# Optimization experiments

Hardware: AMD Instinct MI355X
Metric: run time of the kernel (lower is better)

## Reference

```python
import jax, jax.numpy as jnp
import numpy as np

R_CUTOFF = 5.0
BASIS = 8
NMAX = 8
NSPECIES = 3
EMBED = 16


def _chebyshev_basis(r, r_cutoff, basis_size):
    fc = jnp.where(r < r_cutoff, 0.5 * jnp.cos(jnp.pi * r / r_cutoff) + 0.5, 0.0)
    x = 2.0 * (r / r_cutoff) ** 2 - 1.0
    polys = [jnp.ones_like(x), x]
    for n in range(2, basis_size):
        polys.append(2.0 * x * polys[-1] - polys[-2])
    basis = jnp.stack(polys[:basis_size], axis=-1)  # [E, basis]
    return 0.5 * (basis + 1.0) * fc[:, None]


def setup_inputs() -> dict:
    key = jax.random.key(0)
    ks = jax.random.split(key, 12)
    N, K = 20000, 32
    E = N * K
    positions = jax.random.normal(ks[0], (N, 3), dtype=jnp.float32)
    species = jax.random.randint(ks[1], (N,), 0, NSPECIES, dtype=jnp.int32)
    magmoms = jax.random.normal(ks[2], (N, 3), dtype=jnp.float32)
    # i-major edge list: exactly K edges per atom, grouped by center atom.
    i_idx = jnp.repeat(jnp.arange(N, dtype=jnp.int32), K)
    j_idx = jax.random.randint(ks[3], (E,), 0, N, dtype=jnp.int32)
    edge_index = jnp.stack([i_idx, j_idx], axis=0)
    shifts = jnp.zeros((E, 3), dtype=jnp.float32)
    rb_coefficients = 0.1 * jax.random.normal(ks[4], (NSPECIES * NSPECIES, NMAX, BASIS), dtype=jnp.float32)
    species_embedding = 0.1 * jax.random.normal(ks[5], (NSPECIES, EMBED), dtype=jnp.float32)
    struct_dim = NMAX + NMAX * (NMAX + 1)  # 80
    mag_dim = 3 + 7 * NMAX + 3 * NMAX * NMAX  # 251
    return {
        'positions': positions, 'species': species, 'magmoms': magmoms,
        'edge_index': edge_index, 'shifts': shifts,
        'rb_coefficients': rb_coefficients, 'species_embedding': species_embedding,
        'struct_shift': jnp.zeros(struct_dim, jnp.float32),
        'struct_scale': jnp.ones(struct_dim, jnp.float32),
        'mag_shift': jnp.zeros(mag_dim, jnp.float32),
        'mag_scale': jnp.ones(mag_dim, jnp.float32),
        'atomic_energy_shift': 0.1 * jax.random.normal(ks[6], (NSPECIES,), dtype=jnp.float32),
        'w_struct': 0.05 * jax.random.normal(ks[7], (EMBED + struct_dim,), dtype=jnp.float32),
        'b_struct': 0.05 * jax.random.normal(ks[8], (1,), dtype=jnp.float32),
        'w_mag': 0.05 * jax.random.normal(ks[9], (EMBED + mag_dim,), dtype=jnp.float32),
        'b_mag': 0.05 * jax.random.normal(ks[10], (1,), dtype=jnp.float32),
    }


def _forward(positions, magmoms, shifts, rb_coefficients, species_embedding,
             struct_shift, struct_scale, mag_shift, mag_scale, atomic_energy_shift,
             w_struct, b_struct, w_mag, b_mag, species, edge_index):
    N = positions.shape[0]
    E = edge_index.shape[1]
    K = E // N  # regular neighbor count (edge list is i-major)
    i_idx, j_idx = edge_index[0], edge_index[1]
    r_ij = positions[j_idx] - positions[i_idx] + shifts          # [E,3]
    dist = jnp.linalg.norm(r_ij, axis=-1)                        # [E]
    f_k = _chebyshev_basis(dist, R_CUTOFF, BASIS)                # [E,basis]
    pair_idx = species[i_idx] * NSPECIES + species[j_idx]
    phi = jnp.einsum('enk,ek->en', rb_coefficients[pair_idx], f_k)  # [E,n]
    seg = lambda x: jax.ops.segment_sum(x, i_idx, num_segments=N)
    d = jnp.maximum(dist, 1e-8)[:, None]
    r_hat = r_ij / d
    # --- structural descriptors ---
    d_radial = seg(phi)                                          # [N,n]
    P = seg(phi[:, :, None] * r_hat[:, None, :])                 # [N,n,3]
    PP = jnp.einsum('ina,ima->inm', P, P)
    tu = np.triu_indices(NMAX)
    d_ang_l1 = PP[:, tu[0], tu[1]]
    eye3 = jnp.eye(3, dtype=r_ij.dtype)
    traceless = r_hat[:, :, None] * r_hat[:, None, :] - eye3 / 3.0  # [E,3,3]
    Q = seg(phi[:, :, None, None] * traceless[:, None, :, :])       # [N,n,3,3]
    Qf = Q.reshape(N, NMAX, 9)
    QQ = jnp.einsum('ina,ima->inm', Qf, Qf)
    d_ang_l2 = QQ[:, tu[0], tu[1]]
    desc_struct = jnp.concatenate([d_radial, d_ang_l1, d_ang_l2], axis=-1)
    # --- magnetic descriptors ---
    u = jnp.sum(magmoms * magmoms, axis=-1)                      # [N]
    m_norm = jnp.linalg.norm(magmoms, axis=-1, keepdims=True)
    m_dir = jnp.where(m_norm > 1e-8, magmoms / jnp.maximum(m_norm, 1e-8), 0.0)
    M = seg(phi[:, :, None] * m_dir[j_idx][:, None, :])          # [N,n,3]
    # A_{nm}(i) = sum_{a<b within atom i's edge block} phi_n(a) phi_m(b) (r_a x r_b)
    phi_g = phi.reshape(N, K, NMAX)
    r_g = r_ij.reshape(N, K, 3)
    cross = jnp.cross(r_g[:, :, None, :], r_g[:, None, :, :])    # [N,K,K,3]
    mask = jnp.triu(jnp.ones((K, K), dtype=phi.dtype), k=1)
    tmp = jnp.einsum('iabd,ab,ibm->iamd', cross, mask, phi_g)    # [N,K,3,n]
    A = jnp.einsum('ian,iamd->inmd', phi_g, tmp)                 # [N,n,n,3]
    d_amp = jnp.stack([u, u ** 2, u ** 3], axis=-1)
    d_iso = jnp.sum(m_dir[:, None, :] * M, axis=-1)              # [N,n]
    Qm = jnp.einsum('anij,aj->ani', Q, m_dir)
    d_sia = jnp.sum(m_dir[:, None, :] * Qm, axis=-1)
    mQ = jnp.einsum('ai,amij->amj', m_dir, Q)
    d_sae = jnp.einsum('amj,anj->amn', mQ, M).reshape(N, -1)
    m_cross_M = jnp.cross(jnp.broadcast_to(m_dir[:, None, :], M.shape), M)
    d_dmi = jnp.einsum('inmd,imd->inm', A, m_cross_M).reshape(N, -1)
    u_col = u[:, None]
    d_amp_mix = jnp.concatenate([u_col * d_iso, u_col * d_sia, u_col * d_dmi], axis=-1)
    u_j = u[j_idx]
    d_nbr_amp = seg(phi * u_j[:, None])
    W = seg(phi[:, :, None] * (u_j[:, None] * m_dir[j_idx])[:, None, :])
    d_nbr_amp_ex = jnp.sum(m_dir[:, None, :] * W, axis=-1)
    d_nbr_amp_ex_mix = u_col * d_nbr_amp_ex
    desc_mag = jnp.concatenate([d_amp, d_iso, d_sia, d_sae, d_dmi, d_amp_mix,
                                d_nbr_amp, d_nbr_amp_ex, d_nbr_amp_ex_mix], axis=-1)
    # --- scaling + linear readout heads + per-species shift ---
    ds = (desc_struct - struct_shift) / struct_scale
    dm = (desc_mag - mag_shift) / mag_scale
    emb = species_embedding[species]
    e_struct = jnp.concatenate([emb, ds], axis=-1) @ w_struct + b_struct[0]
    e_mag = jnp.concatenate([emb, dm], axis=-1) @ w_mag + b_mag[0]
    return e_struct + e_mag + atomic_energy_shift[species]        # [N]


def reference(positions, species, magmoms, edge_index, shifts, rb_coefficients,
              species_embedding, struct_shift, struct_scale, mag_shift, mag_scale,
              atomic_energy_shift, w_struct, b_struct, w_mag, b_mag):
    return _forward(positions, magmoms, shifts, rb_coefficients, species_embedding,
                    struct_shift, struct_scale, mag_shift, mag_scale, atomic_energy_shift,
                    w_struct, b_struct, w_mag, b_mag, species, edge_index)
```

## Files before the change

kernel.cpp:

```cpp
#include <hip/hip_runtime.h>

#define NSPEC  3
#define EMBEDD 16
#define KMAX   32
#define RCUT   5.0f
#define PADR   36

__constant__ int TUN[36] = {0,0,0,0,0,0,0,0, 1,1,1,1,1,1,1, 2,2,2,2,2,2, 3,3,3,3,3, 4,4,4,4, 5,5,5, 6,6, 7};
__constant__ int TUM[36] = {0,1,2,3,4,5,6,7, 1,2,3,4,5,6,7, 2,3,4,5,6,7, 3,4,5,6,7, 4,5,6,7, 5,6,7, 6,7, 7};


template<int CTRL, int RMASK, bool BC>
__device__ __forceinline__ float dpp_mov0(float x) {
    return __int_as_float(__builtin_amdgcn_update_dpp(
        0, __float_as_int(x), CTRL, RMASK, 0xF, BC));
}
__device__ __forceinline__ float prefix32(float x) {
    x += dpp_mov0<0x111, 0xF, true >(x);
    x += dpp_mov0<0x112, 0xF, true >(x);
    x += dpp_mov0<0x114, 0xF, true >(x);
    x += dpp_mov0<0x118, 0xF, true >(x);
    x += dpp_mov0<0x142, 0xA, false>(x);
    return x;
}
__device__ __forceinline__ float swz_xor16(float x) {
    return __int_as_float(__builtin_amdgcn_ds_swizzle(__float_as_int(x), 0x401F));
}
__device__ __forceinline__ float red_k4(float x) {
    x += dpp_mov0<0x128, 0xF, true>(x);
    x += swz_xor16(x);
    return x;
}
__device__ __forceinline__ float red32(float x) {
    x += dpp_mov0<0x121, 0xF, true>(x);
    x += dpp_mov0<0x122, 0xF, true>(x);
    x += dpp_mov0<0x124, 0xF, true>(x);
    x += dpp_mov0<0x128, 0xF, true>(x);
    x += swz_xor16(x);
    return x;
}

struct __align__(16) AtomLds {
    float phiT[8 * PADR];
    float tT[8 * PADR];
    float rhx[KMAX], rhy[KMAX], rhz[KMAX];
    float mdx[KMAX], mdy[KMAX], mdz[KMAX];
    float uj[KMAX];
    float P[24], Q[48], M[24], W[24], mQ[24];
};

__global__ __launch_bounds__(256)
void magpot_setup(const float* __restrict__ sshift, const float* __restrict__ sscale,
                  const float* __restrict__ mshift, const float* __restrict__ mscale,
                  const float* __restrict__ wstruct, const float* __restrict__ bstruct,
                  const float* __restrict__ wmag, const float* __restrict__ bmag,
                  float* __restrict__ ws)
{
    __shared__ float red[4];
    const int t = threadIdx.x;
    float c = 0.0f;
    for (int idx = t; idx < 80; idx += 256) {
        const float w = wstruct[16 + idx] / sscale[idx];
        ws[idx] = w;
        c += w * sshift[idx];
    }
    for (int idx = t; idx < 251; idx += 256) {
        const float w = wmag[16 + idx] / mscale[idx];
        ws[80 + idx] = w;
        c += w * mshift[idx];
    }
    if (t < EMBEDD) ws[332 + t] = wstruct[t] + wmag[t];
    #pragma unroll
    for (int d = 1; d <= 32; d <<= 1) c += __shfl_xor(c, d, 64);
    if ((t & 63) == 0) red[t >> 6] = c;
    __syncthreads();
    if (t == 0) ws[331] = bstruct[0] + bmag[0] - (red[0] + red[1] + red[2] + red[3]);
}

__global__ __launch_bounds__(256)
void magpot_main(const float* __restrict__ pos,
                 const int*   __restrict__ species,
                 const float* __restrict__ mag,
                 const int*   __restrict__ eidx,
                 const float* __restrict__ shifts,
                 const float* __restrict__ rb,
                 const float* __restrict__ semb,
                 const float* __restrict__ aes,
                 const float* __restrict__ ws,
                 float* __restrict__ out,
                 int N, int E, int K)
{
    __shared__ AtomLds lds[8];

    const int lane64 = threadIdx.x & 63;
    const int wv     = threadIdx.x >> 6;
    const int h      = lane64 >> 5;
    const int s      = lane64 & 31;
    const int ea     = 31 - s;
    const int i      = blockIdx.x * 8 + wv * 2 + h;
    const bool valid = (i < N);
    const int isafe  = valid ? i : 0;
    AtomLds& L = lds[wv * 2 + h];

    const float* wm = ws + 80;

    const float pix = pos[3*isafe+0], piy = pos[3*isafe+1], piz = pos[3*isafe+2];
    const int   spi = species[isafe];
    const float mgx = mag[3*isafe+0], mgy = mag[3*isafe+1], mgz = mag[3*isafe+2];
    const float u_i = mgx*mgx + mgy*mgy + mgz*mgz;
    const float mn_i = sqrtf(u_i);
    const float mi_inv = (mn_i > 1e-8f) ? (1.0f / mn_i) : 0.0f;
    const float mix = mgx*mi_inv, miy = mgy*mi_inv, miz = mgz*mi_inv;

    float phi[8];
    float rx = 0.0f, ry = 0.0f, rz = 0.0f;
    #pragma unroll
    for (int n = 0; n < 8; ++n) phi[n] = 0.0f;

    if (ea < K) {
        const int e = isafe * K + ea;
        const int j = eidx[E + e];
        rx = pos[3*j+0] - pix + shifts[3*e+0];
        ry = pos[3*j+1] - piy + shifts[3*e+1];
        rz = pos[3*j+2] - piz + shifts[3*e+2];
        const float dist = sqrtf(rx*rx + ry*ry + rz*rz);
        const float fc = (dist < RCUT)
            ? (0.5f * __builtin_amdgcn_cosf(dist * 0.1f) + 0.5f)
            : 0.0f;
        const float xr = dist * (1.0f/RCUT);
        const float x  = 2.0f * xr * xr - 1.0f;
        float f[8];
        {
            float Tm2 = 1.0f, Tm1 = x;
            f[0] = 0.5f * (Tm2 + 1.0f) * fc;
            f[1] = 0.5f * (Tm1 + 1.0f) * fc;
            #pragma unroll
            for (int k = 2; k < 8; ++k) {
                const float T = 2.0f * x * Tm1 - Tm2;
                Tm2 = Tm1; Tm1 = T;
                f[k] = 0.5f * (T + 1.0f) * fc;
            }
        }
        const int spj = species[j];
        const float4* rb4 = (const float4*)(rb + (spi * NSPEC + spj) * 64);
        #pragma unroll
        for (int n = 0; n < 8; ++n) {
            const float4 r0 = rb4[n*2+0];
            const float4 r1 = rb4[n*2+1];
            const float ph = r0.x*f[0] + r0.y*f[1] + r0.z*f[2] + r0.w*f[3]
                           + r1.x*f[4] + r1.y*f[5] + r1.z*f[6] + r1.w*f[7];
            phi[n] = ph;
            L.phiT[n*PADR + ea] = ph;
        }
        const float dinv = 1.0f / fmaxf(dist, 1e-8f);
        L.rhx[ea] = rx * dinv;
        L.rhy[ea] = ry * dinv;
        L.rhz[ea] = rz * dinv;
        const float mjx = mag[3*j+0], mjy = mag[3*j+1], mjz = mag[3*j+2];
        const float uj = mjx*mjx + mjy*mjy + mjz*mjz;
        const float mnj = sqrtf(uj);
        const float mjinv = (mnj > 1e-8f) ? (1.0f / mnj) : 0.0f;
        L.mdx[ea] = mjx * mjinv;
        L.mdy[ea] = mjy * mjinv;
        L.mdz[ea] = mjz * mjinv;
        L.uj[ea] = uj;
    } else {
        #pragma unroll
        for (int n = 0; n < 8; ++n) L.phiT[n*PADR + ea] = 0.0f;
        L.rhx[ea] = 0.0f; L.rhy[ea] = 0.0f; L.rhz[ea] = 0.0f;
        L.mdx[ea] = 0.0f; L.mdy[ea] = 0.0f; L.mdz[ea] = 0.0f;
        L.uj[ea] = 0.0f;
    }
    __syncthreads();

    float p = 0.0f;

    {
        const int k4 = s >> 3;
        const int n  = s & 7;
        const float4* phR = (const float4*)&L.phiT[n*PADR + k4*8];
        const float4* hxR = (const float4*)&L.rhx[k4*8];
        const float4* hyR = (const float4*)&L.rhy[k4*8];
        const float4* hzR = (const float4*)&L.rhz[k4*8];
        const float4* dxR = (const float4*)&L.mdx[k4*8];
        const float4* dyR = (const float4*)&L.mdy[k4*8];
        const float4* dzR = (const float4*)&L.mdz[k4*8];
        const float4* ujR = (const float4*)&L.uj[k4*8];

        float a_dr = 0.0f;
        float aP0 = 0.0f, aP1 = 0.0f, aP2 = 0.0f;
        float aQ0 = 0.0f, aQ1 = 0.0f, aQ2 = 0.0f, aQ3 = 0.0f, aQ4 = 0.0f, aQ5 = 0.0f;
        float aM0 = 0.0f, aM1 = 0.0f, aM2 = 0.0f;
        float a_nb = 0.0f;
        float aW0 = 0.0f, aW1 = 0.0f, aW2 = 0.0f;

        auto acc = [&](float ph, float hx, float hy, float hz,
                       float dx, float dy, float dz, float uj) {
            a_dr += ph;
            aP0 += ph*hx; aP1 += ph*hy; aP2 += ph*hz;
            aQ0 += ph*(hx*hx - (1.0f/3.0f));
            aQ1 += ph*(hx*hy);
            aQ2 += ph*(hx*hz);
            aQ3 += ph*(hy*hy - (1.0f/3.0f));
            aQ4 += ph*(hy*hz);
            aQ5 += ph*(hz*hz - (1.0f/3.0f));
            aM0 += ph*dx; aM1 += ph*dy; aM2 += ph*dz;
            const float pu = ph*uj;
            a_nb += pu;
            aW0 += pu*dx; aW1 += pu*dy; aW2 += pu*dz;
        };
        #pragma unroll
        for (int q = 0; q < 2; ++q) {
            const float4 ph4 = phR[q], hx4 = hxR[q], hy4 = hyR[q], hz4 = hzR[q];
            const float4 dx4 = dxR[q], dy4 = dyR[q], dz4 = dzR[q], uj4 = ujR[q];
            acc(ph4.x, hx4.x, hy4.x, hz4.x, dx4.x, dy4.x, dz4.x, uj4.x);
            acc(ph4.y, hx4.y, hy4.y, hz4.y, dx4.y, dy4.y, dz4.y, uj4.y);
            acc(ph4.z, hx4.z, hy4.z, hz4.z, dx4.z, dy4.z, dz4.z, uj4.z);
            acc(ph4.w, hx4.w, hy4.w, hz4.w, dx4.w, dy4.w, dz4.w, uj4.w);
        }
        a_dr = red_k4(a_dr);
        aP0 = red_k4(aP0); aP1 = red_k4(aP1); aP2 = red_k4(aP2);
        aQ0 = red_k4(aQ0); aQ1 = red_k4(aQ1); aQ2 = red_k4(aQ2);
        aQ3 = red_k4(aQ3); aQ4 = red_k4(aQ4); aQ5 = red_k4(aQ5);
        aM0 = red_k4(aM0); aM1 = red_k4(aM1); aM2 = red_k4(aM2);
        a_nb = red_k4(a_nb);
        aW0 = red_k4(aW0); aW1 = red_k4(aW1); aW2 = red_k4(aW2);

        if (k4 == 0) {
            L.P[n*3+0] = aP0; L.P[n*3+1] = aP1; L.P[n*3+2] = aP2;
            L.Q[n*6+0] = aQ0; L.Q[n*6+1] = aQ1; L.Q[n*6+2] = aQ2;
            L.Q[n*6+3] = aQ3; L.Q[n*6+4] = aQ4; L.Q[n*6+5] = aQ5;
            L.M[n*3+0] = aM0; L.M[n*3+1] = aM1; L.M[n*3+2] = aM2;
            L.W[n*3+0] = aW0; L.W[n*3+1] = aW1; L.W[n*3+2] = aW2;
            p += a_dr * ws[n];
            p += a_nb * wm[227 + n];
        }
        if (s == 8) {
            const float u2 = u_i * u_i;
            p += u_i * wm[0] + u2 * wm[1] + u2 * u_i * wm[2];
        }
        if (s < EMBEDD)
            p += semb[spi * EMBEDD + s] * ws[332 + s];
    }
    __syncthreads();

    #pragma unroll
    for (int c = 0; c < 2; ++c) {
        float wxv[4], wyv[4], wzv[4];
        #pragma unroll
        for (int mm = 0; mm < 4; ++mm) {
            const int m = c*4 + mm;
            const float Mx = L.M[m*3+0], My = L.M[m*3+1], Mz = L.M[m*3+2];
            wxv[mm] = miy*Mz - miz*My;
            wyv[mm] = miz*Mx - mix*Mz;
            wzv[mm] = mix*My - miy*Mx;
        }
        #pragma unroll
        for (int mm = 0; mm < 4; ++mm) {
            const int m = c*4 + mm;
            const float vx = phi[m] * rx;
            const float vy = phi[m] * ry;
            const float vz = phi[m] * rz;
            const float Sx = prefix32(vx) - vx;
            const float Sy = prefix32(vy) - vy;
            const float Sz = prefix32(vz) - vz;
            const float cx = ry*Sz - rz*Sy;
            const float cy = rz*Sx - rx*Sz;
            const float cz = rx*Sy - ry*Sx;
            L.tT[m*PADR + ea] = cx*wxv[mm] + cy*wyv[mm] + cz*wzv[mm];
        }
    }
    __syncthreads();

    {
        const int n  = s >> 2;
        const int mb = (s & 3) << 1;
        const float4* phR = (const float4*)&L.phiT[n*PADR];
        const float4* t0R = (const float4*)&L.tT[mb*PADR];
        const float4* t1R = (const float4*)&L.tT[(mb+1)*PADR];
        float d0 = 0.0f, d1 = 0.0f;
        #pragma unroll
        for (int q = 0; q < 8; ++q) {
            const float4 pv = phR[q];
            const float4 t0 = t0R[q];
            const float4 t1 = t1R[q];
            d0 += pv.x*t0.x + pv.y*t0.y + pv.z*t0.z + pv.w*t0.w;
            d1 += pv.x*t1.x + pv.y*t1.y + pv.z*t1.z + pv.w*t1.w;
        }
        const int i0 = n*8 + mb;
        p += d0 * wm[83 + i0]     + (u_i * d0) * wm[163 + i0];
        p += d1 * wm[83 + i0 + 1] + (u_i * d1) * wm[163 + i0 + 1];
    }

    if (s < 8) {
        const int n = s;
        const float Mx = L.M[n*3+0], My = L.M[n*3+1], Mz = L.M[n*3+2];
        const float diso = mix*Mx + miy*My + miz*Mz;
        const float q0 = L.Q[n*6+0], q1 = L.Q[n*6+1], q2 = L.Q[n*6+2];
        const float q3 = L.Q[n*6+3], q4 = L.Q[n*6+4], q5 = L.Q[n*6+5];
        const float dsia = q0*mix*mix + q3*miy*miy + q5*miz*miz
                         + 2.0f*(q1*mix*miy + q2*mix*miz + q4*miy*miz);
        L.mQ[n*3+0] = q0*mix + q1*miy + q2*miz;
        L.mQ[n*3+1] = q1*mix + q3*miy + q4*miz;
        L.mQ[n*3+2] = q2*mix + q4*miy + q5*miz;
        const float wx = L.W[n*3+0], wy = L.W[n*3+1], wz = L.W[n*3+2];
        const float dnex = mix*wx + miy*wy + miz*wz;
        p += diso * wm[3 + n]  + dsia * wm[11 + n]  + dnex * wm[235 + n]
           + u_i * (diso * wm[147 + n] + dsia * wm[155 + n] + dnex * wm[243 + n]);
    }
    __syncthreads();

    {
        #pragma unroll
        for (int t2 = 0; t2 < 2; ++t2) {
            const int idx = s + t2*32;
            const int m4 = idx >> 3, n4 = idx & 7;
            const float sae = L.mQ[m4*3+0]*L.M[n4*3+0]
                            + L.mQ[m4*3+1]*L.M[n4*3+1]
                            + L.mQ[m4*3+2]*L.M[n4*3+2];
            p += sae * wm[19 + idx];
        }
        #pragma unroll
        for (int t2 = 0; t2 < 2; ++t2) {
            const int idx = s + t2*32;
            if (idx < 36) {
                const int a = TUN[idx], b = TUM[idx];
                const float pp = L.P[a*3+0]*L.P[b*3+0] + L.P[a*3+1]*L.P[b*3+1] + L.P[a*3+2]*L.P[b*3+2];
                const float qq = L.Q[a*6+0]*L.Q[b*6+0] + L.Q[a*6+3]*L.Q[b*6+3] + L.Q[a*6+5]*L.Q[b*6+5]
                       + 2.0f*(L.Q[a*6+1]*L.Q[b*6+1] + L.Q[a*6+2]*L.Q[b*6+2] + L.Q[a*6+4]*L.Q[b*6+4]);
                p += pp * ws[8 + idx] + qq * ws[44 + idx];
            }
        }
    }

    p = red32(p);
    if (s == 0 && valid)
        out[i] = p + ws[331] + aes[spi];
}

extern "C" void kernel_launch(void* const* d_in, const int* in_sizes, int n_in,
                              void* d_out, int out_size, void* d_ws, size_t ws_size,
                              hipStream_t stream) {
    const float* pos     = (const float*)d_in[0];
    const int*   spc     = (const int*)  d_in[1];
    const float* mg      = (const float*)d_in[2];
    const int*   eidx    = (const int*)  d_in[3];
    const float* shf     = (const float*)d_in[4];
    const float* rb      = (const float*)d_in[5];
    const float* semb    = (const float*)d_in[6];
    const float* sshift  = (const float*)d_in[7];
    const float* sscale  = (const float*)d_in[8];
    const float* mshift  = (const float*)d_in[9];
    const float* mscale  = (const float*)d_in[10];
    const float* aes     = (const float*)d_in[11];
    const float* wstruct = (const float*)d_in[12];
    const float* bstruct = (const float*)d_in[13];
    const float* wmag    = (const float*)d_in[14];
    const float* bmag    = (const float*)d_in[15];
    float* out = (float*)d_out;
    float* ws  = (float*)d_ws;

    const int N = in_sizes[1];
    const int E = in_sizes[3] / 2;
    const int K = E / N;

    hipLaunchKernelGGL(magpot_setup, dim3(1), dim3(256), 0, stream,
                       sshift, sscale, mshift, mscale, wstruct, bstruct, wmag, bmag, ws);
    hipLaunchKernelGGL(magpot_main, dim3((N + 7) / 8), dim3(256), 0, stream,
                       pos, spc, mg, eidx, shf, rb, semb, aes, ws, out, N, E, K);
}
```

Measured before the change: 122.1 us.

## Reassociate DMI contraction per edge, drop tT stage and block barriers

Precomputes scaled DMI readout weights transposed in the setup kernel so each edge lane contracts its basis values into per-m coefficients and accumulates the DMI term directly, removing the tT LDS matrix and the phi·t dot-product stage. Isotropic, SIA and exchange terms are computed in the reduction lanes, and LDS arrays are padded to float4. Block-wide __syncthreads are replaced by a wave-local lgkmcnt wait, relying on each atom living within one wavefront. This adds 128 redundant FMAs per lane in exchange for fewer barriers and LDS round trips.

```diff
diff --git a/kernel.cpp b/kernel.cpp
--- a/kernel.cpp
+++ b/kernel.cpp
@@ -40,13 +40,20 @@
     return x;
 }
 
+__device__ __forceinline__ void lds_fence() {
+    asm volatile("s_waitcnt lgkmcnt(0)" ::: "memory");
+}
+
 struct __align__(16) AtomLds {
     float phiT[8 * PADR];
-    float tT[8 * PADR];
     float rhx[KMAX], rhy[KMAX], rhz[KMAX];
     float mdx[KMAX], mdy[KMAX], mdz[KMAX];
     float uj[KMAX];
-    float P[24], Q[48], M[24], W[24], mQ[24];
+    float P4[8*4];
+    float Q8[8*8];
+    float M4[8*4];
+    float mQ4[8*4];
+    float wv4[8*4];
 };
 
 __global__ __launch_bounds__(256)
@@ -70,6 +77,11 @@
         c += w * mshift[idx];
     }
     if (t < EMBEDD) ws[332 + t] = wstruct[t] + wmag[t];
+    if (t < 64) {
+        const int n = t >> 3, m = t & 7;
+        ws[400 + m*8 + n] = wmag[16 + 83 + t]  / mscale[83 + t];
+        ws[464 + m*8 + n] = wmag[16 + 163 + t] / mscale[163 + t];
+    }
     #pragma unroll
     for (int d = 1; d <= 32; d <<= 1) c += __shfl_xor(c, d, 64);
     if ((t & 63) == 0) red[t >> 6] = c;
@@ -171,7 +183,7 @@
         L.mdx[ea] = 0.0f; L.mdy[ea] = 0.0f; L.mdz[ea] = 0.0f;
         L.uj[ea] = 0.0f;
     }
-    __syncthreads();
+    lds_fence();
 
     float p = 0.0f;
 
@@ -227,13 +239,24 @@
         aW0 = red_k4(aW0); aW1 = red_k4(aW1); aW2 = red_k4(aW2);
 
         if (k4 == 0) {
-            L.P[n*3+0] = aP0; L.P[n*3+1] = aP1; L.P[n*3+2] = aP2;
-            L.Q[n*6+0] = aQ0; L.Q[n*6+1] = aQ1; L.Q[n*6+2] = aQ2;
-            L.Q[n*6+3] = aQ3; L.Q[n*6+4] = aQ4; L.Q[n*6+5] = aQ5;
-            L.M[n*3+0] = aM0; L.M[n*3+1] = aM1; L.M[n*3+2] = aM2;
-            L.W[n*3+0] = aW0; L.W[n*3+1] = aW1; L.W[n*3+2] = aW2;
-            p += a_dr * ws[n];
-            p += a_nb * wm[227 + n];
+            ((float4*)L.P4)[n]      = make_float4(aP0, aP1, aP2, 0.0f);
+            ((float4*)L.Q8)[2*n]    = make_float4(aQ0, aQ1, aQ2, aQ3);
+            ((float4*)L.Q8)[2*n+1]  = make_float4(aQ4, aQ5, 0.0f, 0.0f);
+            ((float4*)L.M4)[n]      = make_float4(aM0, aM1, aM2, 0.0f);
+            const float mq0 = aQ0*mix + aQ1*miy + aQ2*miz;
+            const float mq1 = aQ1*mix + aQ3*miy + aQ4*miz;
+            const float mq2 = aQ2*mix + aQ4*miy + aQ5*miz;
+            ((float4*)L.mQ4)[n]     = make_float4(mq0, mq1, mq2, 0.0f);
+            ((float4*)L.wv4)[n]     = make_float4(miy*aM2 - miz*aM1,
+                                                  miz*aM0 - mix*aM2,
+                                                  mix*aM1 - miy*aM0, 0.0f);
+            const float diso = mix*aM0 + miy*aM1 + miz*aM2;
+            const float dsia = aQ0*mix*mix + aQ3*miy*miy + aQ5*miz*miz
+                             + 2.0f*(aQ1*mix*miy + aQ2*mix*miz + aQ4*miy*miz);
+            const float dnex = mix*aW0 + miy*aW1 + miz*aW2;
+            p += a_dr * ws[n] + a_nb * wm[227 + n]
+               + diso * wm[3 + n]  + dsia * wm[11 + n]  + dnex * wm[235 + n]
+               + u_i * (diso * wm[147 + n] + dsia * wm[155 + n] + dnex * wm[243 + n]);
         }
         if (s == 8) {
             const float u2 = u_i * u_i;
@@ -242,22 +265,24 @@
         if (s < EMBEDD)
             p += semb[spi * EMBEDD + s] * ws[332 + s];
     }
-    __syncthreads();
-
-    #pragma unroll
-    for (int c = 0; c < 2; ++c) {
-        float wxv[4], wyv[4], wzv[4];
-        #pragma unroll
-        for (int mm = 0; mm < 4; ++mm) {
-            const int m = c*4 + mm;
-            const float Mx = L.M[m*3+0], My = L.M[m*3+1], Mz = L.M[m*3+2];
-            wxv[mm] = miy*Mz - miz*My;
-            wyv[mm] = miz*Mx - mix*Mz;
-            wzv[mm] = mix*My - miy*Mx;
-        }
-        #pragma unroll
-        for (int mm = 0; mm < 4; ++mm) {
-            const int m = c*4 + mm;
+    lds_fence();
+
+    {
+        float B[8];
+        #pragma unroll
+        for (int m = 0; m < 8; ++m) {
+            float a1 = 0.0f, a2 = 0.0f;
+            #pragma unroll
+            for (int n = 0; n < 8; ++n) {
+                a1 = fmaf(phi[n], ws[400 + m*8 + n], a1);
+                a2 = fmaf(phi[n], ws[464 + m*8 + n], a2);
+            }
+            B[m] = a1 + u_i * a2;
+        }
+        float cdmi = 0.0f;
+        #pragma unroll
+        for (int m = 0; m < 8; ++m) {
+            const float4 wvm = ((const float4*)L.wv4)[m];
             const float vx = phi[m] * rx;
             const float vy = phi[m] * ry;
             const float vz = phi[m] * rz;
@@ -267,67 +292,32 @@
             const float cx = ry*Sz - rz*Sy;
             const float cy = rz*Sx - rx*Sz;
             const float cz = rx*Sy - ry*Sx;
-            L.tT[m*PADR + ea] = cx*wxv[mm] + cy*wyv[mm] + cz*wzv[mm];
-        }
-    }
-    __syncthreads();
-
-    {
-        const int n  = s >> 2;
-        const int mb = (s & 3) << 1;
-        const float4* phR = (const float4*)&L.phiT[n*PADR];
-        const float4* t0R = (const float4*)&L.tT[mb*PADR];
-        const float4* t1R = (const float4*)&L.tT[(mb+1)*PADR];
-        float d0 = 0.0f, d1 = 0.0f;
-        #pragma unroll
-        for (int q = 0; q < 8; ++q) {
-            const float4 pv = phR[q];
-            const float4 t0 = t0R[q];
-            const float4 t1 = t1R[q];
-            d0 += pv.x*t0.x + pv.y*t0.y + pv.z*t0.z + pv.w*t0.w;
-            d1 += pv.x*t1.x + pv.y*t1.y + pv.z*t1.z + pv.w*t1.w;
-        }
-        const int i0 = n*8 + mb;
-        p += d0 * wm[83 + i0]     + (u_i * d0) * wm[163 + i0];
-        p += d1 * wm[83 + i0 + 1] + (u_i * d1) * wm[163 + i0 + 1];
-    }
-
-    if (s < 8) {
-        const int n = s;
-        const float Mx = L.M[n*3+0], My = L.M[n*3+1], Mz = L.M[n*3+2];
-        const float diso = mix*Mx + miy*My + miz*Mz;
-        const float q0 = L.Q[n*6+0], q1 = L.Q[n*6+1], q2 = L.Q[n*6+2];
-        const float q3 = L.Q[n*6+3], q4 = L.Q[n*6+4], q5 = L.Q[n*6+5];
-        const float dsia = q0*mix*mix + q3*miy*miy + q5*miz*miz
-                         + 2.0f*(q1*mix*miy + q2*mix*miz + q4*miy*miz);
-        L.mQ[n*3+0] = q0*mix + q1*miy + q2*miz;
-        L.mQ[n*3+1] = q1*mix + q3*miy + q4*miz;
-        L.mQ[n*3+2] = q2*mix + q4*miy + q5*miz;
-        const float wx = L.W[n*3+0], wy = L.W[n*3+1], wz = L.W[n*3+2];
-        const float dnex = mix*wx + miy*wy + miz*wz;
-        p += diso * wm[3 + n]  + dsia * wm[11 + n]  + dnex * wm[235 + n]
-           + u_i * (diso * wm[147 + n] + dsia * wm[155 + n] + dnex * wm[243 + n]);
-    }
-    __syncthreads();
+            cdmi = fmaf(B[m], cx*wvm.x + cy*wvm.y + cz*wvm.z, cdmi);
+        }
+        p += cdmi;
+    }
 
     {
         #pragma unroll
         for (int t2 = 0; t2 < 2; ++t2) {
             const int idx = s + t2*32;
             const int m4 = idx >> 3, n4 = idx & 7;
-            const float sae = L.mQ[m4*3+0]*L.M[n4*3+0]
-                            + L.mQ[m4*3+1]*L.M[n4*3+1]
-                            + L.mQ[m4*3+2]*L.M[n4*3+2];
-            p += sae * wm[19 + idx];
+            const float4 mQm = ((const float4*)L.mQ4)[m4];
+            const float4 Mn  = ((const float4*)L.M4)[n4];
+            p += (mQm.x*Mn.x + mQm.y*Mn.y + mQm.z*Mn.z) * wm[19 + idx];
         }
         #pragma unroll
         for (int t2 = 0; t2 < 2; ++t2) {
             const int idx = s + t2*32;
             if (idx < 36) {
                 const int a = TUN[idx], b = TUM[idx];
-                const float pp = L.P[a*3+0]*L.P[b*3+0] + L.P[a*3+1]*L.P[b*3+1] + L.P[a*3+2]*L.P[b*3+2];
-                const float qq = L.Q[a*6+0]*L.Q[b*6+0] + L.Q[a*6+3]*L.Q[b*6+3] + L.Q[a*6+5]*L.Q[b*6+5]
-                       + 2.0f*(L.Q[a*6+1]*L.Q[b*6+1] + L.Q[a*6+2]*L.Q[b*6+2] + L.Q[a*6+4]*L.Q[b*6+4]);
+                const float4 Pa = ((const float4*)L.P4)[a];
+                const float4 Pb = ((const float4*)L.P4)[b];
+                const float pp = Pa.x*Pb.x + Pa.y*Pb.y + Pa.z*Pb.z;
+                const float4 Qa0 = ((const float4*)L.Q8)[2*a], Qa1 = ((const float4*)L.Q8)[2*a+1];
+                const float4 Qb0 = ((const float4*)L.Q8)[2*b], Qb1 = ((const float4*)L.Q8)[2*b+1];
+                const float qq = Qa0.x*Qb0.x + Qa0.w*Qb0.w + Qa1.y*Qb1.y
+                       + 2.0f*(Qa0.y*Qb0.y + Qa0.z*Qb0.z + Qa1.x*Qb1.x);
                 p += pp * ws[8 + idx] + qq * ws[44 + idx];
             }
         }
```

After: 123.7 us. No clear change (+1.3%).
